# Performance work log

Hardware: AMD Instinct MI355X
Metric: run time of the kernel (lower is better)

The kernel has to match this reference:

```python
import jax, jax.numpy as jnp
import numpy as np

N_HEAD = 16
RMS_EPS = 1.1920928955078125e-07  # torch F.rms_norm default eps = finfo(fp32).eps


def _rope_tables(seq_len, head_dim, dtype):
    steps = jnp.arange(seq_len, dtype=jnp.float32)
    rates = 10000.0 ** (-jnp.arange(0, head_dim, 2, dtype=jnp.float32) / head_dim)
    angles = jnp.outer(steps, rates)  # [S, D/2]
    return jnp.cos(angles).astype(dtype)[None, None], jnp.sin(angles).astype(dtype)[None, None]


def _apply_rotary(x, cos, sin):
    # interleaved RoPE: pairs (x[2i], x[2i+1]) rotated
    left = x[..., ::2]
    right = x[..., 1::2]
    lo = left * cos - right * sin
    ro = left * sin + right * cos
    return jnp.stack((lo, ro), axis=-1).reshape(x.shape)


def _rms_norm(x, eps=RMS_EPS):
    ms = jnp.mean(jnp.square(x), axis=-1, keepdims=True)
    return x * jax.lax.rsqrt(ms + eps)


def setup_inputs() -> dict:
    key = jax.random.key(0)
    k1, k2, k3 = jax.random.split(key, 3)
    B, S, E = 2, 2048, 2048
    x = jax.random.normal(k1, (B, S, E), dtype=jnp.float32)
    w_qkv = jax.random.normal(k2, (3 * E, E), dtype=jnp.float32) * (E ** -0.5)
    w_proj = jax.random.normal(k3, (E, E), dtype=jnp.float32) * (E ** -0.5)
    return {"x": x, "w_qkv": w_qkv, "w_proj": w_proj}


def reference(x, w_qkv, w_proj):
    B, S, E = x.shape
    H = N_HEAD
    D = E // H

    qkv = x @ w_qkv.T  # [B, S, 3E]
    q, k, v = jnp.split(qkv, 3, axis=-1)
    # [B, S, E] -> [B, H, S, D]
    q = q.reshape(B, S, H, D).transpose(0, 2, 1, 3)
    k = k.reshape(B, S, H, D).transpose(0, 2, 1, 3)
    v = v.reshape(B, S, H, D).transpose(0, 2, 1, 3)

    cos, sin = _rope_tables(S, D, x.dtype)  # [1,1,S,D/2]
    q = _apply_rotary(q, cos, sin)
    k = _apply_rotary(k, cos, sin)

    q = _rms_norm(q)
    k = _rms_norm(k)

    scale = 1.0 / jnp.sqrt(jnp.asarray(D, dtype=x.dtype))
    scores = jnp.einsum("bhqd,bhkd->bhqk", q, k) * scale  # [B,H,S,S]
    causal = jnp.tril(jnp.ones((S, S), dtype=bool))
    scores = jnp.where(causal[None, None], scores, jnp.asarray(-jnp.inf, dtype=scores.dtype))
    attn = jax.nn.softmax(scores, axis=-1)
    y = jnp.einsum("bhqk,bhkd->bhqd", attn, v)  # [B,H,S,D]
    y = y.transpose(0, 2, 1, 3).reshape(B, S, E)
    return y @ w_proj.T
```

## Files before the change

kernel.cpp:

```cpp
#include <hip/hip_runtime.h>

typedef unsigned short ushort_t;
using bf16x8 = __attribute__((ext_vector_type(8))) short;
using u16x8  = __attribute__((ext_vector_type(8))) unsigned short;
using f32x4  = __attribute__((ext_vector_type(4))) float;

#define DEV static __device__ __forceinline__

DEV unsigned short f2bf(float f) {
  union { float f; unsigned u; } a; a.f = f;
  unsigned r = a.u + 0x7fffu + ((a.u >> 16) & 1u);
  return (unsigned short)(r >> 16);
}
DEV float bf2f(unsigned short u) {
  union { unsigned u; float f; } a; a.u = ((unsigned)u) << 16;
  return a.f;
}
DEV void load_lds16(const void* g, void* l) {
  __builtin_amdgcn_global_load_lds(
      (const __attribute__((address_space(1))) void*)g,
      (__attribute__((address_space(3))) void*)l, 16, 0, 0);
}

__global__ __launch_bounds__(256) void cast_kernel(
    const float* __restrict__ src, ushort_t* __restrict__ dst, int n4) {
  int i = blockIdx.x * 256 + threadIdx.x;
  if (i >= n4) return;
  float4 f = ((const float4*)src)[i];
  ushort4 o;
  o.x = f2bf(f.x); o.y = f2bf(f.y); o.z = f2bf(f.z); o.w = f2bf(f.w);
  ((ushort4*)dst)[i] = o;
}

__global__ __launch_bounds__(256) void rope_tables_kernel(float* __restrict__ tab) {
  int idx = blockIdx.x * 256 + threadIdx.x;
  int s = idx >> 6, i = idx & 63;
  float rate = exp2f(-13.287712379549449f * ((float)(2 * i) * (1.0f / 128.0f)));
  float ang = (float)s * rate;
  tab[idx * 2]     = cosf(ang);
  tab[idx * 2 + 1] = sinf(ang);
}

template<int OUTF32>
__global__ __launch_bounds__(256) void gemm_bt(
    const ushort_t* __restrict__ A, const ushort_t* __restrict__ B,
    void* __restrict__ C, int M, int N, int K) {
  __shared__ __align__(16) ushort_t sA[128 * 32];
  __shared__ __align__(16) ushort_t sB[128 * 32];
  const int tid  = threadIdx.x;
  const int wave = tid >> 6;
  const int lane = tid & 63;
  const int lrow = lane & 15;
  const int lk   = lane >> 4;
  const int bm = blockIdx.y * 128;
  const int bn = blockIdx.x * 128;
  const int wrow = (wave >> 1) * 64;
  const int wcol = (wave & 1) * 64;

  f32x4 acc[4][4];
#pragma unroll
  for (int r = 0; r < 4; ++r)
#pragma unroll
    for (int c = 0; c < 4; ++c) acc[r][c] = (f32x4){0.f, 0.f, 0.f, 0.f};

  const int sRow0 = wave * 32 + (lane >> 2);
  const int sRow1 = sRow0 + 16;
  const int sSwz  = ((lane & 3) * 16) ^ ((sRow0 & 3) << 4);
  const char* aS0 = (const char*)A + (size_t)(bm + sRow0) * (size_t)(K * 2) + sSwz;
  const char* aS1 = (const char*)A + (size_t)(bm + sRow1) * (size_t)(K * 2) + sSwz;
  const char* bS0 = (const char*)B + (size_t)(bn + sRow0) * (size_t)(K * 2) + sSwz;
  const char* bS1 = (const char*)B + (size_t)(bn + sRow1) * (size_t)(K * 2) + sSwz;
  char* aD0 = (char*)sA + wave * 2048 + lane * 16;
  char* aD1 = aD0 + 1024;
  char* bD0 = (char*)sB + wave * 2048 + lane * 16;
  char* bD1 = bD0 + 1024;

  int offA[4], offB[4];
  const int fSwz = (lk * 16) ^ ((lrow & 3) << 4);
#pragma unroll
  for (int r = 0; r < 4; ++r) offA[r] = (wrow + r * 16 + lrow) * 64 + fSwz;
#pragma unroll
  for (int c = 0; c < 4; ++c) offB[c] = (wcol + c * 16 + lrow) * 64 + fSwz;

  const int nk = K >> 5;
  for (int ks = 0; ks < nk; ++ks) {
    const size_t koff = (size_t)ks * 64;
    load_lds16(aS0 + koff, aD0);
    load_lds16(aS1 + koff, aD1);
    load_lds16(bS0 + koff, bD0);
    load_lds16(bS1 + koff, bD1);
    __syncthreads();
    bf16x8 af[4], bv[4];
#pragma unroll
    for (int r = 0; r < 4; ++r) af[r] = *(const bf16x8*)((const char*)sA + offA[r]);
#pragma unroll
    for (int c = 0; c < 4; ++c) bv[c] = *(const bf16x8*)((const char*)sB + offB[c]);
#pragma unroll
    for (int r = 0; r < 4; ++r)
#pragma unroll
      for (int c = 0; c < 4; ++c)
        acc[r][c] = __builtin_amdgcn_mfma_f32_16x16x32_bf16(af[r], bv[c], acc[r][c], 0, 0, 0);
    __syncthreads();
  }

#pragma unroll
  for (int r = 0; r < 4; ++r)
#pragma unroll
    for (int i = 0; i < 4; ++i) {
      const size_t row = (size_t)(bm + wrow + r * 16 + lk * 4 + i);
#pragma unroll
      for (int c = 0; c < 4; ++c) {
        const size_t col = (size_t)(bn + wcol + c * 16 + lrow);
        float v = acc[r][c][i];
        if (OUTF32) ((float*)C)[row * (size_t)N + col] = v;
        else        ((ushort_t*)C)[row * (size_t)N + col] = f2bf(v);
      }
    }
}

__global__ __launch_bounds__(256) void rope_rms_kernel(
    const ushort_t* __restrict__ qkv, ushort_t* __restrict__ q,
    ushort_t* __restrict__ k, ushort_t* __restrict__ vt,
    const float* __restrict__ tab) {
  const int lane = threadIdx.x & 63;
  const int row  = blockIdx.x * 4 + (threadIdx.x >> 6);
  const int h = row & 15;
  int t = row >> 4;
  const int which = t % 3; t /= 3;
  const int s = t & 2047;
  const int b = t >> 11;
  const size_t src = ((size_t)(b * 2048 + s)) * 6144 + which * 2048 + h * 128 + lane * 2;
  ushort2 xv = *(const ushort2*)&qkv[src];
  if (which == 2) {
    size_t vbase = ((size_t)((b * 16 + h) * 128 + lane * 2)) * 2048 + s;
    vt[vbase]        = xv.x;
    vt[vbase + 2048] = xv.y;
    return;
  }
  float lo = bf2f(xv.x), ro = bf2f(xv.y);
  const float2 cs = *(const float2*)&tab[(s * 64 + lane) * 2];
  float l2 = lo * cs.x - ro * cs.y;
  float r2 = lo * cs.y + ro * cs.x;
  float ss = l2 * l2 + r2 * r2;
#pragma unroll
  for (int off = 1; off < 64; off <<= 1) ss += __shfl_xor(ss, off);
  float inv = rsqrtf(ss * (1.0f / 128.0f) + 1.1920928955078125e-07f);
  if (which == 0) inv *= 0.1275174398f;
  lo = l2 * inv; ro = r2 * inv;
  ushort_t* dst = (which == 0) ? q : k;
  ushort2 o; o.x = f2bf(lo); o.y = f2bf(ro);
  *(ushort2*)&dst[(((size_t)(b * 16 + h)) * 2048 + s) * 128 + lane * 2] = o;
}

__global__ __launch_bounds__(256) void attn_kernel(
    const ushort_t* __restrict__ Q, const ushort_t* __restrict__ K,
    const ushort_t* __restrict__ VT, ushort_t* __restrict__ Y) {
  __shared__ __align__(16) ushort_t sK[64 * 128];
  __shared__ __align__(16) ushort_t sV[128 * 64];
  const int bh = blockIdx.x;
  const int yp = blockIdx.y;
  const int wave = threadIdx.x >> 6, lane = threadIdx.x & 63;
  const int ql = lane & 15, lk = lane >> 4;
  const size_t hq = (size_t)bh * 2048 * 128;
  const int b = bh >> 4, h = bh & 15;

  const char* kB = (const char*)(K + hq);
  const char* vB = (const char*)(VT + hq);
  const char* kSrc[4]; char* kDst[4];
  const char* vSrc[4]; char* vDst[4];
#pragma unroll
  for (int t = 0; t < 4; ++t) {
    int r = wave * 16 + t * 4 + (lane >> 4);
    int kgr = r >> 4, lkr = (r >> 2) & 3, ir = r & 3;
    int rho = (kgr >> 1) * 32 + lkr * 8 + (kgr & 1) * 4 + ir;
    kSrc[t] = kB + rho * 256 + (((lane & 15) * 16) ^ ((r & 7) << 4));
    kDst[t] = (char*)sK + (wave * 256 + t * 64 + lane) * 16;
    int d = wave * 32 + t * 8 + (lane >> 3);
    vSrc[t] = vB + (size_t)d * 4096 + (((lane & 7) * 16) ^ ((d & 7) << 4));
    vDst[t] = (char*)sV + (wave * 256 + t * 64 + lane) * 16;
  }

  for (int pass = 0; pass < 2; ++pass) {
    const int qt = pass ? (31 - yp) : yp;
    const int q = qt * 64 + wave * 16 + ql;

    bf16x8 qf[4];
#pragma unroll
    for (int ks = 0; ks < 4; ++ks)
      qf[ks] = *(const bf16x8*)&Q[hq + (size_t)q * 128 + ks * 32 + lk * 8];

    f32x4 acc[8];
#pragma unroll
    for (int g = 0; g < 8; ++g) acc[g] = (f32x4){0.f, 0.f, 0.f, 0.f};
    float mrow = -3.0e38f, lsum = 0.f;

    for (int kt = 0; kt <= qt; ++kt) {
#pragma unroll
      for (int t = 0; t < 4; ++t) {
        load_lds16(kSrc[t] + (size_t)kt * 16384, kDst[t]);
        load_lds16(vSrc[t] + kt * 128, vDst[t]);
      }
      __syncthreads();

      f32x4 st[4];
#pragma unroll
      for (int kg = 0; kg < 4; ++kg) st[kg] = (f32x4){0.f, 0.f, 0.f, 0.f};
#pragma unroll
      for (int kg = 0; kg < 4; ++kg) {
        const int row = kg * 16 + ql;
        const int rswz = (row & 7) << 4;
#pragma unroll
        for (int ks = 0; ks < 4; ++ks) {
          bf16x8 kf = *(const bf16x8*)((const char*)sK + row * 256 + ((ks * 64 + lk * 16) ^ rswz));
          st[kg] = __builtin_amdgcn_mfma_f32_16x16x32_bf16(kf, qf[ks], st[kg], 0, 0, 0);
        }
      }
      float sv[4][4]; float mp = -3.0e38f;
#pragma unroll
      for (int kg = 0; kg < 4; ++kg) {
        const int kl = ((kg >> 1) << 5) + lk * 8 + ((kg & 1) << 2);
#pragma unroll
        for (int i = 0; i < 4; ++i) {
          const int key = kt * 64 + kl + i;
          float v = (key <= q) ? st[kg][i] : -3.0e38f;
          sv[kg][i] = v;
          mp = fmaxf(mp, v);
        }
      }
      mp = fmaxf(mp, __shfl_xor(mp, 16));
      mp = fmaxf(mp, __shfl_xor(mp, 32));
      const float mn = fmaxf(mrow, mp);
      const float corr = exp2f(mrow - mn);
      mrow = mn;
      float p[4][4]; float rs = 0.f;
#pragma unroll
      for (int kg = 0; kg < 4; ++kg)
#pragma unroll
        for (int i = 0; i < 4; ++i) {
          float e = exp2f(sv[kg][i] - mn);
          p[kg][i] = e; rs += e;
        }
      rs += __shfl_xor(rs, 16);
      rs += __shfl_xor(rs, 32);
      lsum = lsum * corr + rs;
#pragma unroll
      for (int g = 0; g < 8; ++g)
#pragma unroll
        for (int i = 0; i < 4; ++i) acc[g][i] *= corr;
      bf16x8 pb[2];
#pragma unroll
      for (int c = 0; c < 2; ++c) {
        union { bf16x8 v; ushort_t u[8]; } pk;
#pragma unroll
        for (int j = 0; j < 8; ++j) pk.u[j] = f2bf(p[2 * c + (j >> 2)][j & 3]);
        pb[c] = pk.v;
      }
#pragma unroll
      for (int dg = 0; dg < 8; ++dg) {
        const int d = dg * 16 + ql;
        const int dswz = (d & 7) << 4;
#pragma unroll
        for (int c = 0; c < 2; ++c) {
          bf16x8 vf = *(const bf16x8*)((const char*)sV + d * 128 + ((c * 64 + lk * 16) ^ dswz));
          acc[dg] = __builtin_amdgcn_mfma_f32_16x16x32_bf16(vf, pb[c], acc[dg], 0, 0, 0);
        }
      }
      __syncthreads();
    }

    const float inv = 1.0f / lsum;
    const size_t orow = ((size_t)(b * 2048 + q)) * 2048 + h * 128;
#pragma unroll
    for (int dg = 0; dg < 8; ++dg) {
      ushort4 o;
      o.x = f2bf(acc[dg][0] * inv);
      o.y = f2bf(acc[dg][1] * inv);
      o.z = f2bf(acc[dg][2] * inv);
      o.w = f2bf(acc[dg][3] * inv);
      *(ushort4*)&Y[orow + dg * 16 + lk * 4] = o;
    }
  }
}

extern "C" void kernel_launch(void* const* d_in, const int* in_sizes, int n_in,
                              void* d_out, int out_size, void* d_ws, size_t ws_size,
                              hipStream_t stream) {
  const float* x     = (const float*)d_in[0];
  const float* wqkv  = (const float*)d_in[1];
  const float* wproj = (const float*)d_in[2];
  float* out = (float*)d_out;
  char* ws = (char*)d_ws;

  ushort_t* x_bf     = (ushort_t*)(ws);
  ushort_t* wqkv_bf  = (ushort_t*)(ws + 16777216);
  ushort_t* wproj_bf = (ushort_t*)(ws + 41943040);
  ushort_t* qkv_bf   = (ushort_t*)(ws + 50331648);
  ushort_t* q_bf     = (ushort_t*)(ws + 100663296);
  ushort_t* k_bf     = (ushort_t*)(ws + 117440512);
  ushort_t* vt_bf    = (ushort_t*)(ws + 134217728);
  float*    tab      = (float*)(ws + 150994944);
  if (ws_size < 152043520u) return;

  cast_kernel<<<8192, 256, 0, stream>>>(x, x_bf, 2097152);
  cast_kernel<<<12288, 256, 0, stream>>>(wqkv, wqkv_bf, 3145728);
  cast_kernel<<<4096, 256, 0, stream>>>(wproj, wproj_bf, 1048576);
  rope_tables_kernel<<<512, 256, 0, stream>>>(tab);

  gemm_bt<0><<<dim3(48, 32), 256, 0, stream>>>(x_bf, wqkv_bf, qkv_bf, 4096, 6144, 2048);

  rope_rms_kernel<<<49152, 256, 0, stream>>>(qkv_bf, q_bf, k_bf, vt_bf, tab);

  attn_kernel<<<dim3(32, 16), 256, 0, stream>>>(q_bf, k_bf, vt_bf, qkv_bf );

  gemm_bt<1><<<dim3(16, 32), 256, 0, stream>>>(qkv_bf, wproj_bf, out, 4096, 2048, 2048);
}
```

Before: 344.7 us.

## Replace GEMM with 256-row tiles, 4-slot async LDS pipeline and XCD-aware block remap

Replaces the 128x128 single-buffered GEMM with a 512-thread kernel using 256xBN tiles and a four-slot LDS ring. Global-to-LDS loads for three future k-steps stay in flight behind explicit vmcnt waits. A workgroup id remap is meant to spread neighbouring tiles across the chiplets for better L2 reuse, and setprio raises priority around the MFMA burst. The aim is to hide load latency and raise operand reuse, at the cost of more LDS and registers per block, fewer blocks in flight, and hand-coded waitcnt counts that depend on exact load ordering.

```diff
diff --git a/kernel.cpp b/kernel.cpp
--- a/kernel.cpp
+++ b/kernel.cpp
@@ -41,77 +41,105 @@
   tab[idx * 2 + 1] = sinf(ang);
 }
 
-template<int OUTF32>
-__global__ __launch_bounds__(256) void gemm_bt(
+template<int BN, int OUTF32>
+__global__ __launch_bounds__(512) void gemm8p(
     const ushort_t* __restrict__ A, const ushort_t* __restrict__ B,
     void* __restrict__ C, int M, int N, int K) {
-  __shared__ __align__(16) ushort_t sA[128 * 32];
-  __shared__ __align__(16) ushort_t sB[128 * 32];
-  const int tid  = threadIdx.x;
-  const int wave = tid >> 6;
-  const int lane = tid & 63;
-  const int lrow = lane & 15;
-  const int lk   = lane >> 4;
-  const int bm = blockIdx.y * 128;
-  const int bn = blockIdx.x * 128;
-  const int wrow = (wave >> 1) * 64;
-  const int wcol = (wave & 1) * 64;
-
-  f32x4 acc[4][4];
-#pragma unroll
-  for (int r = 0; r < 4; ++r)
-#pragma unroll
-    for (int c = 0; c < 4; ++c) acc[r][c] = (f32x4){0.f, 0.f, 0.f, 0.f};
-
-  const int sRow0 = wave * 32 + (lane >> 2);
-  const int sRow1 = sRow0 + 16;
-  const int sSwz  = ((lane & 3) * 16) ^ ((sRow0 & 3) << 4);
-  const char* aS0 = (const char*)A + (size_t)(bm + sRow0) * (size_t)(K * 2) + sSwz;
-  const char* aS1 = (const char*)A + (size_t)(bm + sRow1) * (size_t)(K * 2) + sSwz;
-  const char* bS0 = (const char*)B + (size_t)(bn + sRow0) * (size_t)(K * 2) + sSwz;
-  const char* bS1 = (const char*)B + (size_t)(bn + sRow1) * (size_t)(K * 2) + sSwz;
-  char* aD0 = (char*)sA + wave * 2048 + lane * 16;
-  char* aD1 = aD0 + 1024;
-  char* bD0 = (char*)sB + wave * 2048 + lane * 16;
-  char* bD1 = bD0 + 1024;
-
-  int offA[4], offB[4];
-  const int fSwz = (lk * 16) ^ ((lrow & 3) << 4);
-#pragma unroll
-  for (int r = 0; r < 4; ++r) offA[r] = (wrow + r * 16 + lrow) * 64 + fSwz;
-#pragma unroll
-  for (int c = 0; c < 4; ++c) offB[c] = (wcol + c * 16 + lrow) * 64 + fSwz;
-
-  const int nk = K >> 5;
-  for (int ks = 0; ks < nk; ++ks) {
-    const size_t koff = (size_t)ks * 64;
-    load_lds16(aS0 + koff, aD0);
-    load_lds16(aS1 + koff, aD1);
-    load_lds16(bS0 + koff, bD0);
-    load_lds16(bS1 + koff, bD1);
-    __syncthreads();
-    bf16x8 af[4], bv[4];
-#pragma unroll
-    for (int r = 0; r < 4; ++r) af[r] = *(const bf16x8*)((const char*)sA + offA[r]);
-#pragma unroll
-    for (int c = 0; c < 4; ++c) bv[c] = *(const bf16x8*)((const char*)sB + offB[c]);
-#pragma unroll
-    for (int r = 0; r < 4; ++r)
-#pragma unroll
-      for (int c = 0; c < 4; ++c)
-        acc[r][c] = __builtin_amdgcn_mfma_f32_16x16x32_bf16(af[r], bv[c], acc[r][c], 0, 0, 0);
-    __syncthreads();
+  constexpr int NF      = BN / 64;
+  constexpr int NSPAN   = BN / 4;
+  constexpr int SLOT_A  = 256 * 32;
+  constexpr int SLOT_B  = BN * 32;
+  constexpr int SLOT    = SLOT_A + SLOT_B;
+  constexpr int LOADS_B = BN / 128;
+  constexpr int VMC     = (2 + LOADS_B) * 3;
+  __shared__ __align__(16) ushort_t lds[4 * SLOT];
+
+  const int nby = M >> 8;
+  const int nbx = N / BN;
+  const int nwg = nby * nbx;
+  const int orig = blockIdx.x;
+  const int wgid = (orig & 7) * (nwg >> 3) + (orig >> 3);
+  const int by = wgid % nby;
+  const int bx = wgid / nby;
+  const int bm = by * 256, bn = bx * BN;
+
+  const int tid = threadIdx.x;
+  const int wave = tid >> 6, lane = tid & 63;
+  const int ql = lane & 15, lk = lane >> 4;
+  const int wm = wave >> 2, wn = wave & 3;
+
+  f32x4 acc[8][NF];
+#pragma unroll
+  for (int m = 0; m < 8; ++m)
+#pragma unroll
+    for (int n = 0; n < NF; ++n) acc[m][n] = (f32x4){0.f, 0.f, 0.f, 0.f};
+
+  const int srow = tid >> 2;
+  const int scol = (tid & 3) * 16;
+  const int sswz = scol ^ (((srow >> 1) & 3) << 4);
+  const size_t rbA = (size_t)(K * 2);
+  const char* aS0 = (const char*)A + (size_t)(bm + srow) * rbA + sswz;
+  const char* aS1 = (const char*)A + (size_t)(bm + srow + 128) * rbA + sswz;
+  const char* bS0 = (const char*)B + (size_t)(bn + srow) * rbA + sswz;
+  const char* bS1 = (const char*)B + (size_t)(bn + srow + 128) * rbA + sswz;
+  char* ldsc = (char*)lds;
+  const int dA0 = tid * 16;
+  const int dA1 = tid * 16 + 8192;
+  const int dB0 = SLOT_A * 2 + tid * 16;
+  const int dB1 = SLOT_A * 2 + tid * 16 + 8192;
+
+#define ISSUE(KS, SL) do {                                   \
+    const size_t ko = (size_t)(KS) * 64;                     \
+    char* sb = ldsc + (SL) * (SLOT * 2);                     \
+    load_lds16(aS0 + ko, sb + dA0);                          \
+    load_lds16(aS1 + ko, sb + dA1);                          \
+    load_lds16(bS0 + ko, sb + dB0);                          \
+    if (LOADS_B == 2) load_lds16(bS1 + ko, sb + dB1);        \
+  } while (0)
+
+  const int qswz = ((ql >> 1) & 3) << 4;
+  const int fcol = (lk * 16) ^ qswz;
+  const int aOff = (wm * 128 + ql) * 64 + fcol;
+  const int bOff = SLOT_A * 2 + (wn * NSPAN + ql) * 64 + fcol;
+
+  const int ns = K >> 5;
+  ISSUE(0, 0); ISSUE(1, 1); ISSUE(2, 2);
+
+  for (int s = 0; s < ns; ++s) {
+    int kn = s + 3; if (kn >= ns) kn = ns - 1;
+    ISSUE(kn, (s + 3) & 3);
+    if (VMC == 12) asm volatile("s_waitcnt vmcnt(12)" ::: "memory");
+    else           asm volatile("s_waitcnt vmcnt(9)"  ::: "memory");
+    asm volatile("s_barrier" ::: "memory");
+
+    const char* sb = ldsc + (s & 3) * (SLOT * 2);
+    bf16x8 af[8], bfr[NF];
+#pragma unroll
+    for (int m = 0; m < 8; ++m) af[m] = *(const bf16x8*)(sb + aOff + m * 1024);
+#pragma unroll
+    for (int n = 0; n < NF; ++n) bfr[n] = *(const bf16x8*)(sb + bOff + n * 1024);
+
+    __builtin_amdgcn_s_setprio(1);
+#pragma unroll
+    for (int m = 0; m < 8; ++m)
+#pragma unroll
+      for (int n = 0; n < NF; ++n)
+        acc[m][n] = __builtin_amdgcn_mfma_f32_16x16x32_bf16(af[m], bfr[n], acc[m][n], 0, 0, 0);
+    __builtin_amdgcn_s_setprio(0);
+    asm volatile("s_barrier" ::: "memory");
   }
-
-#pragma unroll
-  for (int r = 0; r < 4; ++r)
+  asm volatile("s_waitcnt vmcnt(0)" ::: "memory");
+#undef ISSUE
+
+#pragma unroll
+  for (int m = 0; m < 8; ++m)
 #pragma unroll
     for (int i = 0; i < 4; ++i) {
-      const size_t row = (size_t)(bm + wrow + r * 16 + lk * 4 + i);
-#pragma unroll
-      for (int c = 0; c < 4; ++c) {
-        const size_t col = (size_t)(bn + wcol + c * 16 + lrow);
-        float v = acc[r][c][i];
+      const size_t row = (size_t)(bm + wm * 128 + m * 16 + lk * 4 + i);
+#pragma unroll
+      for (int n = 0; n < NF; ++n) {
+        const size_t col = (size_t)(bn + wn * NSPAN + n * 16 + ql);
+        float v = acc[m][n][i];
         if (OUTF32) ((float*)C)[row * (size_t)N + col] = v;
         else        ((ushort_t*)C)[row * (size_t)N + col] = f2bf(v);
       }
@@ -306,11 +334,11 @@
   cast_kernel<<<4096, 256, 0, stream>>>(wproj, wproj_bf, 1048576);
   rope_tables_kernel<<<512, 256, 0, stream>>>(tab);
 
-  gemm_bt<0><<<dim3(48, 32), 256, 0, stream>>>(x_bf, wqkv_bf, qkv_bf, 4096, 6144, 2048);
+  gemm8p<256, 0><<<384, 512, 0, stream>>>(x_bf, wqkv_bf, qkv_bf, 4096, 6144, 2048);
 
   rope_rms_kernel<<<49152, 256, 0, stream>>>(qkv_bf, q_bf, k_bf, vt_bf, tab);
 
   attn_kernel<<<dim3(32, 16), 256, 0, stream>>>(q_bf, k_bf, vt_bf, qkv_bf );
 
-  gemm_bt<1><<<dim3(16, 32), 256, 0, stream>>>(qkv_bf, wproj_bf, out, 4096, 2048, 2048);
-}
+  gemm8p<128, 1><<<256, 512, 0, stream>>>(qkv_bf, wproj_bf, out, 4096, 2048, 2048);
+}
```

Measured after the change: 317.8 us. 1.08x faster.

## Replace GEMMs with larger-tile triple-buffered pipelined MFMA kernel

Applied to the files above, without the earlier changes.

Replaces the simple single-buffer 128x128 GEMM with a templated 256-wide tile kernel using 512 threads, a three-stage LDS ring fed by direct global-to-LDS loads, and split A/B staging interleaved with MFMA phases under raised wave priority. It also remaps workgroup IDs in an XCD-aware order and uses a different LDS swizzle. The aim is to hide global load latency and raise data reuse per tile for both the QKV and output projections. In exchange it needs much more LDS per block (one block per CU), more barriers per iteration, and it launches far fewer blocks.

```diff
diff --git a/kernel.cpp b/kernel.cpp
--- a/kernel.cpp
+++ b/kernel.cpp
@@ -2,7 +2,6 @@
 
 typedef unsigned short ushort_t;
 using bf16x8 = __attribute__((ext_vector_type(8))) short;
-using u16x8  = __attribute__((ext_vector_type(8))) unsigned short;
 using f32x4  = __attribute__((ext_vector_type(4))) float;
 
 #define DEV static __device__ __forceinline__
@@ -41,77 +40,142 @@
   tab[idx * 2 + 1] = sinf(ang);
 }
 
-template<int OUTF32>
-__global__ __launch_bounds__(256) void gemm_bt(
-    const ushort_t* __restrict__ A, const ushort_t* __restrict__ B,
+template<int BM, int BN, int WM, int WN, int OUTF32>
+__global__ __launch_bounds__(512, 1) void gemm3b(
+    const ushort_t* __restrict__ A, const ushort_t* __restrict__ Bm,
     void* __restrict__ C, int M, int N, int K) {
-  __shared__ __align__(16) ushort_t sA[128 * 32];
-  __shared__ __align__(16) ushort_t sB[128 * 32];
+  constexpr int MF   = BM / WM / 16;
+  constexpr int NF   = BN / WN / 16;
+  constexpr int ABY  = BM * 64;
+  constexpr int BBY  = BN * 64;
+  constexpr int BUFB = ABY + BBY;
+  constexpr int LA   = ABY / 8192;
+  constexpr int LB   = BBY / 8192;
+  constexpr int L    = LA + LB;
+  __shared__ __align__(16) char lds[3 * BUFB];
+
+  const int nby = M / BM;
+  const int nwg = nby * (N / BN);
+  const int orig = blockIdx.x;
+  const int wgid = (orig & 7) * (nwg >> 3) + (orig >> 3);
+  const int bm = (wgid % nby) * BM;
+  const int bn = (wgid / nby) * BN;
+
   const int tid  = threadIdx.x;
+  const int lane = tid & 63;
   const int wave = tid >> 6;
-  const int lane = tid & 63;
-  const int lrow = lane & 15;
-  const int lk   = lane >> 4;
-  const int bm = blockIdx.y * 128;
-  const int bn = blockIdx.x * 128;
-  const int wrow = (wave >> 1) * 64;
-  const int wcol = (wave & 1) * 64;
-
-  f32x4 acc[4][4];
-#pragma unroll
-  for (int r = 0; r < 4; ++r)
-#pragma unroll
-    for (int c = 0; c < 4; ++c) acc[r][c] = (f32x4){0.f, 0.f, 0.f, 0.f};
-
-  const int sRow0 = wave * 32 + (lane >> 2);
-  const int sRow1 = sRow0 + 16;
-  const int sSwz  = ((lane & 3) * 16) ^ ((sRow0 & 3) << 4);
-  const char* aS0 = (const char*)A + (size_t)(bm + sRow0) * (size_t)(K * 2) + sSwz;
-  const char* aS1 = (const char*)A + (size_t)(bm + sRow1) * (size_t)(K * 2) + sSwz;
-  const char* bS0 = (const char*)B + (size_t)(bn + sRow0) * (size_t)(K * 2) + sSwz;
-  const char* bS1 = (const char*)B + (size_t)(bn + sRow1) * (size_t)(K * 2) + sSwz;
-  char* aD0 = (char*)sA + wave * 2048 + lane * 16;
-  char* aD1 = aD0 + 1024;
-  char* bD0 = (char*)sB + wave * 2048 + lane * 16;
-  char* bD1 = bD0 + 1024;
-
-  int offA[4], offB[4];
-  const int fSwz = (lk * 16) ^ ((lrow & 3) << 4);
-#pragma unroll
-  for (int r = 0; r < 4; ++r) offA[r] = (wrow + r * 16 + lrow) * 64 + fSwz;
-#pragma unroll
-  for (int c = 0; c < 4; ++c) offB[c] = (wcol + c * 16 + lrow) * 64 + fSwz;
-
-  const int nk = K >> 5;
-  for (int ks = 0; ks < nk; ++ks) {
-    const size_t koff = (size_t)ks * 64;
-    load_lds16(aS0 + koff, aD0);
-    load_lds16(aS1 + koff, aD1);
-    load_lds16(bS0 + koff, bD0);
-    load_lds16(bS1 + koff, bD1);
-    __syncthreads();
-    bf16x8 af[4], bv[4];
-#pragma unroll
-    for (int r = 0; r < 4; ++r) af[r] = *(const bf16x8*)((const char*)sA + offA[r]);
-#pragma unroll
-    for (int c = 0; c < 4; ++c) bv[c] = *(const bf16x8*)((const char*)sB + offB[c]);
-#pragma unroll
-    for (int r = 0; r < 4; ++r)
-#pragma unroll
-      for (int c = 0; c < 4; ++c)
-        acc[r][c] = __builtin_amdgcn_mfma_f32_16x16x32_bf16(af[r], bv[c], acc[r][c], 0, 0, 0);
-    __syncthreads();
-  }
-
-#pragma unroll
-  for (int r = 0; r < 4; ++r)
+  const int ql = lane & 15, lk = lane >> 4;
+  const int wm = wave / WN, wn = wave % WN;
+
+  f32x4 acc[MF][NF];
+#pragma unroll
+  for (int m = 0; m < MF; ++m)
+#pragma unroll
+    for (int n = 0; n < NF; ++n) acc[m][n] = (f32x4){0.f, 0.f, 0.f, 0.f};
+
+  const size_t rb = (size_t)K * 2;
+  const char* srcA[LA]; const char* srcB[LB];
+#pragma unroll
+  for (int l = 0; l < LA; ++l) {
+    const int r = l * 128 + (tid >> 2);
+    const int slot = (tid & 3) ^ ((r >> 1) & 3);
+    srcA[l] = (const char*)A + (size_t)(bm + r) * rb + slot * 16;
+  }
+#pragma unroll
+  for (int l = 0; l < LB; ++l) {
+    const int r = l * 128 + (tid >> 2);
+    const int slot = (tid & 3) ^ ((r >> 1) & 3);
+    srcB[l] = (const char*)Bm + (size_t)(bn + r) * rb + slot * 16;
+  }
+  char* const ldsc = (char*)lds;
+  const int dT = tid * 16;
+
+  int aOff[MF], bOff[NF];
+#pragma unroll
+  for (int m = 0; m < MF; ++m) {
+    const int r = wm * (BM / WM) + m * 16 + ql;
+    aOff[m] = r * 64 + ((lk ^ ((r >> 1) & 3)) * 16);
+  }
+#pragma unroll
+  for (int n = 0; n < NF; ++n) {
+    const int r = wn * (BN / WN) + n * 16 + ql;
+    bOff[n] = ABY + r * 64 + ((lk ^ ((r >> 1) & 3)) * 16);
+  }
+
+#define STAGE_A(SB, KT) do {                                        \
+    _Pragma("unroll")                                               \
+    for (int l = 0; l < LA; ++l)                                    \
+      load_lds16(srcA[l] + (size_t)(KT) * 64, (SB) + l * 8192 + dT);\
+  } while (0)
+#define STAGE_B(SB, KT) do {                                        \
+    _Pragma("unroll")                                               \
+    for (int l = 0; l < LB; ++l)                                    \
+      load_lds16(srcB[l] + (size_t)(KT) * 64, (SB) + ABY + l * 8192 + dT); \
+  } while (0)
+#define MFMA(a, b, c) __builtin_amdgcn_mfma_f32_16x16x32_bf16(a, b, c, 0, 0, 0)
+
+  const int ns = K >> 5;
+
+  STAGE_A(ldsc, 0); STAGE_B(ldsc, 0);
+  STAGE_A(ldsc + BUFB, 1); STAGE_B(ldsc + BUFB, 1);
+  asm volatile("s_waitcnt vmcnt(%0)" :: "n"(L) : "memory");
+  __builtin_amdgcn_s_barrier();
+
+  int cbi = 0;
+  for (int t = 0; t < ns; ++t) {
+    const char* cb = ldsc + cbi * BUFB;
+    const int sbi = (cbi + 2 >= 3) ? cbi - 1 : cbi + 2;
+    char* sb = ldsc + sbi * BUFB;
+    const int kt2 = (t + 2 < ns) ? t + 2 : ns - 1;
+
+    bf16x8 aF[MF], bF[NF];
+#pragma unroll
+    for (int m = 0; m < MF; ++m) aF[m] = *(const bf16x8*)(cb + aOff[m]);
+#pragma unroll
+    for (int n = 0; n < NF / 2; ++n) bF[n] = *(const bf16x8*)(cb + bOff[n]);
+    asm volatile("" ::: "memory");
+    STAGE_A(sb, kt2);
+    __builtin_amdgcn_s_barrier();
+    __builtin_amdgcn_s_setprio(1);
+#pragma unroll
+    for (int n = 0; n < NF / 2; ++n)
+#pragma unroll
+      for (int m = 0; m < MF; ++m)
+        acc[m][n] = MFMA(aF[m], bF[n], acc[m][n]);
+    __builtin_amdgcn_s_setprio(0);
+    __builtin_amdgcn_s_barrier();
+
+#pragma unroll
+    for (int n = NF / 2; n < NF; ++n) bF[n] = *(const bf16x8*)(cb + bOff[n]);
+    asm volatile("" ::: "memory");
+    STAGE_B(sb, kt2);
+    asm volatile("s_waitcnt vmcnt(%0)" :: "n"(L) : "memory");
+    __builtin_amdgcn_s_barrier();
+    __builtin_amdgcn_s_setprio(1);
+#pragma unroll
+    for (int n = NF / 2; n < NF; ++n)
+#pragma unroll
+      for (int m = 0; m < MF; ++m)
+        acc[m][n] = MFMA(aF[m], bF[n], acc[m][n]);
+    __builtin_amdgcn_s_setprio(0);
+    __builtin_amdgcn_s_barrier();
+
+    cbi = (cbi + 1 >= 3) ? 0 : cbi + 1;
+  }
+  asm volatile("s_waitcnt vmcnt(0)" ::: "memory");
+#undef STAGE_A
+#undef STAGE_B
+#undef MFMA
+
+#pragma unroll
+  for (int m = 0; m < MF; ++m)
 #pragma unroll
     for (int i = 0; i < 4; ++i) {
-      const size_t row = (size_t)(bm + wrow + r * 16 + lk * 4 + i);
-#pragma unroll
-      for (int c = 0; c < 4; ++c) {
-        const size_t col = (size_t)(bn + wcol + c * 16 + lrow);
-        float v = acc[r][c][i];
+      const size_t row = (size_t)(bm + wm * (BM / WM) + m * 16 + lk * 4 + i);
+#pragma unroll
+      for (int n = 0; n < NF; ++n) {
+        const size_t col = (size_t)(bn + wn * (BN / WN) + n * 16 + ql);
+        float v = acc[m][n][i];
         if (OUTF32) ((float*)C)[row * (size_t)N + col] = v;
         else        ((ushort_t*)C)[row * (size_t)N + col] = f2bf(v);
       }
@@ -306,11 +370,11 @@
   cast_kernel<<<4096, 256, 0, stream>>>(wproj, wproj_bf, 1048576);
   rope_tables_kernel<<<512, 256, 0, stream>>>(tab);
 
-  gemm_bt<0><<<dim3(48, 32), 256, 0, stream>>>(x_bf, wqkv_bf, qkv_bf, 4096, 6144, 2048);
+  gemm3b<256, 256, 2, 4, 0><<<384, 512, 0, stream>>>(x_bf, wqkv_bf, qkv_bf, 4096, 6144, 2048);
 
   rope_rms_kernel<<<49152, 256, 0, stream>>>(qkv_bf, q_bf, k_bf, vt_bf, tab);
 
   attn_kernel<<<dim3(32, 16), 256, 0, stream>>>(q_bf, k_bf, vt_bf, qkv_bf );
 
-  gemm_bt<1><<<dim3(16, 32), 256, 0, stream>>>(qkv_bf, wproj_bf, out, 4096, 2048, 2048);
-}
+  gemm3b<256, 128, 4, 2, 1><<<256, 512, 0, stream>>>(qkv_bf, wproj_bf, out, 4096, 2048, 2048);
+}
```

After: 313.1 us. -9.2%, faster.
